# Optimization experiments

Hardware: AMD Instinct MI355X
Metric: run time of the kernel (lower is better)

Reference implementation:

```python
import jax, jax.numpy as jnp
import numpy as np

B, T, D = 64, 512, 1536   # batch, time, enc_size (2*768)
H = 30                    # z_rnn_size
L_SUP, R_SUP = -0.1, 1.1  # HardKuma stretched support
EPS = 1e-5


def setup_inputs() -> dict:
    key = jax.random.key(0)
    ks = jax.random.split(key, 12)
    s = 0.02
    return {
        "x": jax.random.normal(ks[0], (B, T, D), dtype=jnp.float32),
        "u": jax.random.uniform(ks[1], (B, T, 1), dtype=jnp.float32),
        # LSTMCell(enc_size + 1 -> H), torch gate order [i, f, g, o]
        "Wih": jax.random.normal(ks[2], (4 * H, D + 1), dtype=jnp.float32) * s,
        "Whh": jax.random.normal(ks[3], (4 * H, H), dtype=jnp.float32) * s,
        "bih": jax.random.normal(ks[4], (4 * H,), dtype=jnp.float32) * s,
        "bhh": jax.random.normal(ks[5], (4 * H,), dtype=jnp.float32) * s,
        # KumaGate: Linear(D + H -> 1) + Softplus for a and b
        "Wa": jax.random.normal(ks[6], (1, D + H), dtype=jnp.float32) * s,
        "ba": jax.random.normal(ks[7], (1,), dtype=jnp.float32) * s,
        "Wb": jax.random.normal(ks[8], (1, D + H), dtype=jnp.float32) * s,
        "bb": jax.random.normal(ks[9], (1,), dtype=jnp.float32) * s,
    }


def reference(x, u, Wih, Whh, bih, bhh, Wa, ba, Wb, bb):
    # x: [B, T, D], u: [B, T, 1] uniform reparam noise
    hseq = jnp.swapaxes(x, 0, 1)               # [T, B, D]
    useq = jnp.swapaxes(u, 0, 1)               # [T, B, 1]
    batch = x.shape[0]

    def step(carry, inp):
        hx, cx = carry                          # [B, H] each
        h_t, u_t = inp                          # [B, D], [B, 1]
        feat = jnp.concatenate([h_t, hx], axis=-1)          # [B, D+H]
        a = jnp.clip(jax.nn.softplus(feat @ Wa.T + ba), 1e-6, 100.0)
        b = jnp.clip(jax.nn.softplus(feat @ Wb.T + bb), 1e-6, 100.0)
        # HardKuma reparameterized sample (training branch)
        uu = jnp.clip(u_t, EPS, 1.0 - EPS)
        s = (1.0 - (1.0 - uu) ** (1.0 / b)) ** (1.0 / a)     # Kuma icdf
        t = s * (R_SUP - L_SUP) + L_SUP                      # stretch
        z_t = jnp.clip(t, 0.0, 1.0)                          # hard rectify, [B, 1]
        # LSTMCell update (torch gate order i, f, g, o)
        rnn_in = jnp.concatenate([h_t, z_t], axis=-1)        # [B, D+1]
        gates = rnn_in @ Wih.T + bih + hx @ Whh.T + bhh      # [B, 4H]
        i, f, g, o = jnp.split(gates, 4, axis=-1)
        c_new = jax.nn.sigmoid(f) * cx + jax.nn.sigmoid(i) * jnp.tanh(g)
        h_new = jax.nn.sigmoid(o) * jnp.tanh(c_new)
        return (h_new, c_new), z_t

    init = (jnp.zeros((batch, H), x.dtype), jnp.zeros((batch, H), x.dtype))
    _, zs = jax.lax.scan(step, init, (hseq, useq))           # zs: [T, B, 1]
    return jnp.swapaxes(zs[..., 0], 0, 1)                    # [B, T]
```

## Files before the change

### kernel.cpp

```cpp
#include <hip/hip_runtime.h>
#include <math.h>

#define Bb 64
#define Tt 512
#define Dd 1536
#define Hh 30
#define NC 128
#define Mm (Bb*Tt)
#define KSTEPS 48

typedef unsigned short u16;
typedef __attribute__((ext_vector_type(8))) short short8v;
typedef __attribute__((ext_vector_type(4))) float f32x4;

__device__ __forceinline__ float rcpf_(float x) { return __builtin_amdgcn_rcpf(x); }
__device__ __forceinline__ float sigmoidf_(float x) {
    return rcpf_(1.f + __expf(-x));
}
__device__ __forceinline__ float tanhf_fast(float x) {
    float e = __expf(2.f * x);
    return fmaf(-2.f, rcpf_(e + 1.f), 1.f);
}
__device__ __forceinline__ float softplus_(float x) {
    return fmaxf(x, 0.f) + __logf(1.f + __expf(-fabsf(x)));
}
__device__ __forceinline__ float rl_f(float v, int lane) {
    return __uint_as_float(__builtin_amdgcn_readlane(__float_as_uint(v), lane));
}

#define QPERM(src, CTRL) \
    __uint_as_float((unsigned)__builtin_amdgcn_mov_dpp((int)__float_as_uint(src), CTRL, 0xF, 0xF, false))

__device__ __forceinline__ f32x4 mm_bf16(short8v a, short8v b, f32x4 c) {
    return __builtin_amdgcn_mfma_f32_16x16x32_bf16(a, b, c, 0, 0, 0);
}

union U4S8 { unsigned int u[4]; short8v s; };

__device__ __forceinline__ void cvt_split(const float4 a, const float4 b,
                                          short8v& hi, short8v& lo) {
    float x[8] = {a.x, a.y, a.z, a.w, b.x, b.y, b.z, b.w};
    U4S8 H, L;
#pragma unroll
    for (int i = 0; i < 4; i++) {
        unsigned int u0 = __float_as_uint(x[2 * i]);
        unsigned int u1 = __float_as_uint(x[2 * i + 1]);
        unsigned int h0 = u0 & 0xffff0000u;
        unsigned int h1 = u1 & 0xffff0000u;
        H.u[i] = (u0 >> 16) | h1;
        float l0 = x[2 * i]     - __uint_as_float(h0);
        float l1 = x[2 * i + 1] - __uint_as_float(h1);
        L.u[i] = (__float_as_uint(l0) >> 16) | (__float_as_uint(l1) & 0xffff0000u);
    }
    hi = H.s;
    lo = L.s;
}

__global__ __launch_bounds__(256) void pack_w(const float* __restrict__ Wih,
                                              const float* __restrict__ Wa,
                                              const float* __restrict__ Wb,
                                              u16* __restrict__ Wbh,
                                              u16* __restrict__ Wbl) {
    const int k = blockIdx.x * 256 + threadIdx.x;
    const int c = blockIdx.y;
    float v = 0.f;
    if (c < 120)       v = Wih[c * (Dd + 1) + k];
    else if (c == 120) v = Wa[k];
    else if (c == 121) v = Wb[k];
    unsigned int u = __float_as_uint(v);
    unsigned int h = u & 0xffff0000u;
    float lo = v - __uint_as_float(h);
    Wbh[(size_t)c * Dd + k] = (u16)(u >> 16);
    Wbl[(size_t)c * Dd + k] = (u16)(__float_as_uint(lo) >> 16);
}

__global__ __launch_bounds__(64) void pack_s3(const float* __restrict__ Wih,
                                              const float* __restrict__ Whh,
                                              const float* __restrict__ Wa,
                                              const float* __restrict__ Wb,
                                              float* __restrict__ WS3) {
    const int l = threadIdx.x;
    const int q = l >> 2, g = l & 3;
    float v0[32], v1[32];
#pragma unroll
    for (int j = 0; j < 32; j++) { v0[j] = 0.f; v1[j] = 0.f; }
    {
        int c0 = g * 30 + q;
        for (int j = 0; j < 30; j++) v0[j] = Whh[c0 * Hh + j];
        v0[30] = Wih[c0 * (Dd + 1) + Dd];
    }
    if (q < 14) {
        int c1 = g * 30 + 16 + q;
        for (int j = 0; j < 30; j++) v1[j] = Whh[c1 * Hh + j];
        v1[30] = Wih[c1 * (Dd + 1) + Dd];
    } else if (l == 56) {
        for (int j = 0; j < 30; j++) v1[j] = Wa[Dd + j];
    } else if (l == 60) {
        for (int j = 0; j < 30; j++) v1[j] = Wb[Dd + j];
    }
    float* dst = WS3 + (size_t)l * 64;
    for (int j = 0; j < 32; j++) { dst[j] = v0[j]; dst[32 + j] = v1[j]; }
}

__global__ __launch_bounds__(256, 2) void gemm_k(const float* __restrict__ X,
                                                 const u16* __restrict__ Wbh,
                                                 const u16* __restrict__ Wbl,
                                                 const float* __restrict__ bih,
                                                 const float* __restrict__ bhh,
                                                 const float* __restrict__ ba,
                                                 const float* __restrict__ bbp,
                                                 float* __restrict__ GX) {
    const int t    = threadIdx.x;
    const int lane = t & 63;
    const int wid  = t >> 6;
    const int wrow = wid >> 1;
    const int wcol = wid & 1;
    const int m0   = blockIdx.x * 64 + wrow * 32;
    const int n0   = wcol * 64;
    const int lr   = lane & 15;
    const int lk   = lane >> 4;

    const float* xa0 = X + (size_t)(m0 + lr) * Dd + lk * 8;
    const float* xa1 = xa0 + (size_t)16 * Dd;
    const u16*   pbh = Wbh + (size_t)(n0 + lr) * Dd + lk * 8;
    const u16*   pbl = Wbl + (size_t)(n0 + lr) * Dd + lk * 8;

    f32x4 acc[2][4];
#pragma unroll
    for (int nt = 0; nt < 4; nt++) {
        int c = n0 + nt * 16 + lr;
        float bv = (c < 120) ? (bih[c] + bhh[c])
                 : (c == 120) ? ba[0]
                 : (c == 121) ? bbp[0] : 0.f;
        f32x4 v = {bv, bv, bv, bv};
        acc[0][nt] = v;
        acc[1][nt] = v;
    }

#define LOADA(ra, ks) do {                                        \
        ra[0] = *(const float4*)(xa0 + (ks) * 32);                \
        ra[1] = *(const float4*)(xa0 + (ks) * 32 + 4);            \
        ra[2] = *(const float4*)(xa1 + (ks) * 32);                \
        ra[3] = *(const float4*)(xa1 + (ks) * 32 + 4);            \
    } while (0)

#define LOADB(bh, bl, ks) do {                                               \
        _Pragma("unroll")                                                    \
        for (int nt = 0; nt < 4; nt++) {                                     \
            bh[nt] = *(const short8v*)(pbh + (size_t)nt * 16 * Dd + (ks) * 32); \
            bl[nt] = *(const short8v*)(pbl + (size_t)nt * 16 * Dd + (ks) * 32); \
        }                                                                    \
    } while (0)

#define STEP(ra, bh, bl) do {                                     \
        short8v ah0, al0, ah1, al1;                               \
        cvt_split(ra[0], ra[1], ah0, al0);                        \
        cvt_split(ra[2], ra[3], ah1, al1);                        \
        _Pragma("unroll")                                         \
        for (int nt = 0; nt < 4; nt++)                            \
            acc[0][nt] = mm_bf16(ah0, bh[nt], acc[0][nt]);        \
        _Pragma("unroll")                                         \
        for (int nt = 0; nt < 4; nt++)                            \
            acc[1][nt] = mm_bf16(ah1, bh[nt], acc[1][nt]);        \
        _Pragma("unroll")                                         \
        for (int nt = 0; nt < 4; nt++)                            \
            acc[0][nt] = mm_bf16(al0, bh[nt], acc[0][nt]);        \
        _Pragma("unroll")                                         \
        for (int nt = 0; nt < 4; nt++)                            \
            acc[1][nt] = mm_bf16(al1, bh[nt], acc[1][nt]);        \
        _Pragma("unroll")                                         \
        for (int nt = 0; nt < 4; nt++)                            \
            acc[0][nt] = mm_bf16(ah0, bl[nt], acc[0][nt]);        \
        _Pragma("unroll")                                         \
        for (int nt = 0; nt < 4; nt++)                            \
            acc[1][nt] = mm_bf16(ah1, bl[nt], acc[1][nt]);        \
    } while (0)

    float4  ra0[4], ra1[4];
    short8v bh0[4], bl0[4], bh1[4], bl1[4];

    LOADA(ra0, 0);
    LOADB(bh0, bl0, 0);
    int ks = 0;
    for (; ks < KSTEPS - 2; ks += 2) {
        LOADA(ra1, ks + 1);
        LOADB(bh1, bl1, ks + 1);
        STEP(ra0, bh0, bl0);
        LOADA(ra0, ks + 2);
        LOADB(bh0, bl0, ks + 2);
        STEP(ra1, bh1, bl1);
    }
    LOADA(ra1, KSTEPS - 1);
    LOADB(bh1, bl1, KSTEPS - 1);
    STEP(ra0, bh0, bl0);
    STEP(ra1, bh1, bl1);

#undef LOADA
#undef LOADB
#undef STEP

#pragma unroll
    for (int mt = 0; mt < 2; mt++)
#pragma unroll
        for (int nt = 0; nt < 4; nt++) {
            float* dst = GX + (size_t)(m0 + mt * 16 + lk * 4) * NC + n0 + nt * 16 + lr;
#pragma unroll
            for (int r = 0; r < 4; r++)
                dst[(size_t)r * NC] = acc[mt][nt][r];
        }
}

#define PIN16(A, B) asm volatile("" \
    : "+v"(A[B+0]), "+v"(A[B+1]), "+v"(A[B+2]),  "+v"(A[B+3]),  "+v"(A[B+4]),  "+v"(A[B+5]),  "+v"(A[B+6]),  "+v"(A[B+7]), \
      "+v"(A[B+8]), "+v"(A[B+9]), "+v"(A[B+10]), "+v"(A[B+11]), "+v"(A[B+12]), "+v"(A[B+13]), "+v"(A[B+14]), "+v"(A[B+15]))

__global__
__attribute__((amdgpu_flat_work_group_size(64, 64)))
__attribute__((amdgpu_waves_per_eu(1)))
void scan_k(const float* __restrict__ u,
            const float* __restrict__ gx,
            const float* __restrict__ WS3,
            float* __restrict__ out) {
    __shared__ float lus[Tt];
    __shared__ float zbuf[Tt];
    const int b = blockIdx.x;
    const int l = threadIdx.x;
    const int q = l >> 2, g = l & 3;

    for (int k = l; k < Tt; k += 64) {
        float uu = u[b * Tt + k];
        uu = fminf(fmaxf(uu, 1e-5f), 1.f - 1e-5f);
        lus[k] = __logf(1.f - uu);
    }
    __syncthreads();

    float wv0[32], wv1[32];
    {
        const float* wp = WS3 + (size_t)l * 64;
#pragma unroll
        for (int j = 0; j < 8; j++) {
            float4 a4 = ((const float4*)wp)[j];
            float4 b4 = ((const float4*)(wp + 32))[j];
            wv0[4 * j + 0] = a4.x; wv0[4 * j + 1] = a4.y;
            wv0[4 * j + 2] = a4.z; wv0[4 * j + 3] = a4.w;
            wv1[4 * j + 0] = b4.x; wv1[4 * j + 1] = b4.y;
            wv1[4 * j + 2] = b4.z; wv1[4 * j + 3] = b4.w;
        }
    }

    const int c0 = g * 30 + q;
    const int c1 = (q < 14) ? (g * 30 + 16 + q) : ((l == 56) ? 120 : (l == 60) ? 121 : 124);
    const float* p0 = gx + (size_t)b * Tt * NC + c0;
    const float* p1 = gx + (size_t)b * Tt * NC + c1;

    float hs[Hh];
#pragma unroll
    for (int k = 0; k < Hh; k++) hs[k] = 0.f;
    float cst0 = 0.f, cst1 = 0.f;

    float A0 = p0[0], B0 = p1[0];
    float A1 = p0[NC], B1 = p1[NC];
    float lu0 = lus[0], lu1 = lus[1];

    for (int t = 0; t < Tt; t++) {
        PIN16(wv0, 0); PIN16(wv0, 16);
        PIN16(wv1, 0); PIN16(wv1, 16);

        float d10 = B0, d11 = 0.f, d12 = 0.f, d13 = 0.f;
#pragma unroll
        for (int k = 0; k < 28; k += 4) {
            d10 = fmaf(wv1[k], hs[k], d10);         d11 = fmaf(wv1[k + 1], hs[k + 1], d11);
            d12 = fmaf(wv1[k + 2], hs[k + 2], d12); d13 = fmaf(wv1[k + 3], hs[k + 3], d13);
        }
        d10 = fmaf(wv1[28], hs[28], d10); d11 = fmaf(wv1[29], hs[29], d11);
        float dot1 = (d10 + d12) + (d11 + d13);

        const float av = rl_f(dot1, 56);
        const float bv = rl_f(dot1, 60);
        float a  = fminf(fmaxf(softplus_(av), 1e-6f), 100.f);
        float bk = fminf(fmaxf(softplus_(bv), 1e-6f), 100.f);
        float lu = lu0;
        float p = __expf(lu * rcpf_(bk));
        float inner = 1.f - p;
        float s = (inner <= 0.f) ? 0.f : __expf(__logf(inner) * rcpf_(a));
        float z = fminf(fmaxf(fmaf(1.2f, s, -0.1f), 0.f), 1.f);

        float d00 = A0, d01 = 0.f, d02 = 0.f, d03 = 0.f;
#pragma unroll
        for (int k = 0; k < 28; k += 4) {
            d00 = fmaf(wv0[k], hs[k], d00);         d01 = fmaf(wv0[k + 1], hs[k + 1], d01);
            d02 = fmaf(wv0[k + 2], hs[k + 2], d02); d03 = fmaf(wv0[k + 3], hs[k + 3], d03);
        }
        d00 = fmaf(wv0[28], hs[28], d00); d01 = fmaf(wv0[29], hs[29], d01);
        float dot0 = (d00 + d02) + (d01 + d03);

        A0 = A1; B0 = B1; lu0 = lu1;
        if (t + 2 < Tt) {
            A1 = p0[(size_t)(t + 2) * NC];
            B1 = p1[(size_t)(t + 2) * NC];
            lu1 = lus[t + 2];
        }

        float acc0 = fmaf(z, wv0[30], dot0);
        float acc1 = fmaf(z, wv1[30], dot1);

        float val0 = (g == 2) ? tanhf_fast(acc0) : sigmoidf_(acc0);
        float val1 = (g == 2) ? tanhf_fast(acc1) : sigmoidf_(acc1);

        float vf0 = QPERM(val0, 0x55), vg0 = QPERM(val0, 0xAA), vo0 = QPERM(val0, 0xFF);
        float vf1 = QPERM(val1, 0x55), vg1 = QPERM(val1, 0xAA), vo1 = QPERM(val1, 0xFF);

        float cn0 = fmaf(vf0, cst0, val0 * vg0);
        float hn0 = vo0 * tanhf_fast(cn0);
        cst0 = cn0;
        float cn1 = fmaf(vf1, cst1, val1 * vg1);
        float hn1 = vo1 * tanhf_fast(cn1);
        cst1 = cn1;

#pragma unroll
        for (int k = 0; k < 16; k++) hs[k] = rl_f(hn0, 4 * k);
#pragma unroll
        for (int k = 16; k < Hh; k++) hs[k] = rl_f(hn1, 4 * (k - 16));

        if (l == 0) zbuf[t] = z;
    }
    __syncthreads();
    for (int k = l; k < Tt; k += 64) out[b * Tt + k] = zbuf[k];
}

extern "C" void kernel_launch(void* const* d_in, const int* in_sizes, int n_in,
                              void* d_out, int out_size, void* d_ws, size_t ws_size,
                              hipStream_t stream) {
    const float* x   = (const float*)d_in[0];
    const float* u   = (const float*)d_in[1];
    const float* Wih = (const float*)d_in[2];
    const float* Whh = (const float*)d_in[3];
    const float* bih = (const float*)d_in[4];
    const float* bhh = (const float*)d_in[5];
    const float* Wa  = (const float*)d_in[6];
    const float* ba  = (const float*)d_in[7];
    const float* Wb  = (const float*)d_in[8];
    const float* bbp = (const float*)d_in[9];
    float* out = (float*)d_out;

    char* wsb = (char*)d_ws;
    u16*   Wbh = (u16*)(wsb);
    u16*   Wbl = (u16*)(wsb + 393216);
    float* WS3 = (float*)(wsb + 786432);
    float* GX  = (float*)(wsb + 802816);

    pack_w<<<dim3(Dd / 256, NC), 256, 0, stream>>>(Wih, Wa, Wb, Wbh, Wbl);
    pack_s3<<<1, 64, 0, stream>>>(Wih, Whh, Wa, Wb, WS3);
    gemm_k<<<Mm / 64, 256, 0, stream>>>(x, Wbh, Wbl, bih, bhh, ba, bbp, GX);
    scan_k<<<Bb, 64, 0, stream>>>(u, GX, WS3, out);
}
```

Baseline: 666.4 us.

## Stream gate projections into LDS in double-buffered chunks via async global_load_lds

The recurrent scan kernel used to issue scattered per-step global loads of the precomputed gate inputs, two steps ahead. It now copies 32-timestep chunks of the gate projections into a double-buffered shared-memory tile with asynchronous global-to-LDS loads, so each step reads from LDS with short latency. The per-step gate activation is also merged into one exp-plus-reciprocal path, with a per-lane multiplier selecting between sigmoid and tanh. This costs 32KB of LDS and a full vmcnt wait at each chunk boundary, and there is no barrier between the async LDS write and the reads, which relies on a single-wave workgroup.

```diff
diff --git a/kernel.cpp b/kernel.cpp
--- a/kernel.cpp
+++ b/kernel.cpp
@@ -30,6 +30,10 @@
 
 #define QPERM(src, CTRL) \
     __uint_as_float((unsigned)__builtin_amdgcn_mov_dpp((int)__float_as_uint(src), CTRL, 0xF, 0xF, false))
+
+#define GLOAD_LDS16(gp, lp) \
+    __builtin_amdgcn_global_load_lds((const __attribute__((address_space(1))) void*)(const void*)(gp), \
+                                     (__attribute__((address_space(3))) void*)(void*)(lp), 16, 0, 0)
 
 __device__ __forceinline__ f32x4 mm_bf16(short8v a, short8v b, f32x4 c) {
     return __builtin_amdgcn_mfma_f32_16x16x32_bf16(a, b, c, 0, 0, 0);
@@ -223,6 +227,7 @@
             float* __restrict__ out) {
     __shared__ float lus[Tt];
     __shared__ float zbuf[Tt];
+    __shared__ float gxs[2][32][NC];
     const int b = blockIdx.x;
     const int l = threadIdx.x;
     const int q = l >> 2, g = l & 3;
@@ -250,79 +255,104 @@
 
     const int c0 = g * 30 + q;
     const int c1 = (q < 14) ? (g * 30 + 16 + q) : ((l == 56) ? 120 : (l == 60) ? 121 : 124);
-    const float* p0 = gx + (size_t)b * Tt * NC + c0;
-    const float* p1 = gx + (size_t)b * Tt * NC + c1;
+    const float* gxb0 = gx + (size_t)b * Tt * NC;
+
+    const float mge = (g == 2) ? 2.f : -1.f;
 
     float hs[Hh];
 #pragma unroll
     for (int k = 0; k < Hh; k++) hs[k] = 0.f;
     float cst0 = 0.f, cst1 = 0.f;
 
-    float A0 = p0[0], B0 = p1[0];
-    float A1 = p0[NC], B1 = p1[NC];
-    float lu0 = lus[0], lu1 = lus[1];
-
-    for (int t = 0; t < Tt; t++) {
-        PIN16(wv0, 0); PIN16(wv0, 16);
-        PIN16(wv1, 0); PIN16(wv1, 16);
-
-        float d10 = B0, d11 = 0.f, d12 = 0.f, d13 = 0.f;
-#pragma unroll
-        for (int k = 0; k < 28; k += 4) {
-            d10 = fmaf(wv1[k], hs[k], d10);         d11 = fmaf(wv1[k + 1], hs[k + 1], d11);
-            d12 = fmaf(wv1[k + 2], hs[k + 2], d12); d13 = fmaf(wv1[k + 3], hs[k + 3], d13);
+#pragma unroll
+    for (int j = 0; j < 16; j++)
+        GLOAD_LDS16(gxb0 + j * 256 + l * 4, &gxs[0][0][0] + j * 256);
+    asm volatile("s_waitcnt vmcnt(0)" ::: "memory");
+    float A0 = gxs[0][0][c0], B0 = gxs[0][0][c1], L0 = lus[0];
+
+    for (int c = 0; c < Tt / 32; c++) {
+        if (c < Tt / 32 - 1) {
+            const float* gch = gxb0 + (size_t)(c + 1) * 32 * NC;
+            float* lch = &gxs[(c + 1) & 1][0][0];
+#pragma unroll
+            for (int j = 0; j < 16; j++)
+                GLOAD_LDS16(gch + j * 256 + l * 4, lch + j * 256);
         }
-        d10 = fmaf(wv1[28], hs[28], d10); d11 = fmaf(wv1[29], hs[29], d11);
-        float dot1 = (d10 + d12) + (d11 + d13);
-
-        const float av = rl_f(dot1, 56);
-        const float bv = rl_f(dot1, 60);
-        float a  = fminf(fmaxf(softplus_(av), 1e-6f), 100.f);
-        float bk = fminf(fmaxf(softplus_(bv), 1e-6f), 100.f);
-        float lu = lu0;
-        float p = __expf(lu * rcpf_(bk));
-        float inner = 1.f - p;
-        float s = (inner <= 0.f) ? 0.f : __expf(__logf(inner) * rcpf_(a));
-        float z = fminf(fmaxf(fmaf(1.2f, s, -0.1f), 0.f), 1.f);
-
-        float d00 = A0, d01 = 0.f, d02 = 0.f, d03 = 0.f;
-#pragma unroll
-        for (int k = 0; k < 28; k += 4) {
-            d00 = fmaf(wv0[k], hs[k], d00);         d01 = fmaf(wv0[k + 1], hs[k + 1], d01);
-            d02 = fmaf(wv0[k + 2], hs[k + 2], d02); d03 = fmaf(wv0[k + 3], hs[k + 3], d03);
+#pragma unroll 1
+        for (int s = 0; s < 32; s++) {
+            const int t = c * 32 + s;
+            PIN16(wv0, 0); PIN16(wv0, 16);
+            PIN16(wv1, 0); PIN16(wv1, 16);
+
+            float A1 = 0.f, B1 = 0.f, L1 = 0.f;
+            if (t + 1 < Tt) {
+                if (s < 31) {
+                    A1 = gxs[c & 1][s + 1][c0];
+                    B1 = gxs[c & 1][s + 1][c1];
+                } else {
+                    asm volatile("s_waitcnt vmcnt(0)" ::: "memory");
+                    A1 = gxs[(c + 1) & 1][0][c0];
+                    B1 = gxs[(c + 1) & 1][0][c1];
+                }
+                L1 = lus[t + 1];
+            }
+
+            float d10 = B0, d11 = 0.f, d12 = 0.f, d13 = 0.f;
+#pragma unroll
+            for (int k = 0; k < 28; k += 4) {
+                d10 = fmaf(wv1[k], hs[k], d10);         d11 = fmaf(wv1[k + 1], hs[k + 1], d11);
+                d12 = fmaf(wv1[k + 2], hs[k + 2], d12); d13 = fmaf(wv1[k + 3], hs[k + 3], d13);
+            }
+            d10 = fmaf(wv1[28], hs[28], d10); d11 = fmaf(wv1[29], hs[29], d11);
+            float dot1 = (d10 + d12) + (d11 + d13);
+
+            const float av = rl_f(dot1, 56);
+            const float bv = rl_f(dot1, 60);
+            float a  = fminf(fmaxf(softplus_(av), 1e-6f), 100.f);
+            float bk = fminf(fmaxf(softplus_(bv), 1e-6f), 100.f);
+            float lu = L0;
+            float p = __expf(lu * rcpf_(bk));
+            float inner = 1.f - p;
+            float sK = (inner <= 0.f) ? 0.f : __expf(__logf(inner) * rcpf_(a));
+            float z = fminf(fmaxf(fmaf(1.2f, sK, -0.1f), 0.f), 1.f);
+
+            float d00 = A0, d01 = 0.f, d02 = 0.f, d03 = 0.f;
+#pragma unroll
+            for (int k = 0; k < 28; k += 4) {
+                d00 = fmaf(wv0[k], hs[k], d00);         d01 = fmaf(wv0[k + 1], hs[k + 1], d01);
+                d02 = fmaf(wv0[k + 2], hs[k + 2], d02); d03 = fmaf(wv0[k + 3], hs[k + 3], d03);
+            }
+            d00 = fmaf(wv0[28], hs[28], d00); d01 = fmaf(wv0[29], hs[29], d01);
+            float dot0 = (d00 + d02) + (d01 + d03);
+
+            float acc0 = fmaf(z, wv0[30], dot0);
+            float acc1 = fmaf(z, wv1[30], dot1);
+
+            float e0 = __expf(acc0 * mge);
+            float e1 = __expf(acc1 * mge);
+            float r0 = rcpf_(1.f + e0);
+            float r1 = rcpf_(1.f + e1);
+            float val0 = (g == 2) ? fmaf(-2.f, r0, 1.f) : r0;
+            float val1 = (g == 2) ? fmaf(-2.f, r1, 1.f) : r1;
+
+            float vf0 = QPERM(val0, 0x55), vg0 = QPERM(val0, 0xAA), vo0 = QPERM(val0, 0xFF);
+            float vf1 = QPERM(val1, 0x55), vg1 = QPERM(val1, 0xAA), vo1 = QPERM(val1, 0xFF);
+
+            float cn0 = fmaf(vf0, cst0, val0 * vg0);
+            float hn0 = vo0 * tanhf_fast(cn0);
+            cst0 = cn0;
+            float cn1 = fmaf(vf1, cst1, val1 * vg1);
+            float hn1 = vo1 * tanhf_fast(cn1);
+            cst1 = cn1;
+
+#pragma unroll
+            for (int k = 0; k < 16; k++) hs[k] = rl_f(hn0, 4 * k);
+#pragma unroll
+            for (int k = 16; k < Hh; k++) hs[k] = rl_f(hn1, 4 * (k - 16));
+
+            if (l == 0) zbuf[t] = z;
+            A0 = A1; B0 = B1; L0 = L1;
         }
-        d00 = fmaf(wv0[28], hs[28], d00); d01 = fmaf(wv0[29], hs[29], d01);
-        float dot0 = (d00 + d02) + (d01 + d03);
-
-        A0 = A1; B0 = B1; lu0 = lu1;
-        if (t + 2 < Tt) {
-            A1 = p0[(size_t)(t + 2) * NC];
-            B1 = p1[(size_t)(t + 2) * NC];
-            lu1 = lus[t + 2];
-        }
-
-        float acc0 = fmaf(z, wv0[30], dot0);
-        float acc1 = fmaf(z, wv1[30], dot1);
-
-        float val0 = (g == 2) ? tanhf_fast(acc0) : sigmoidf_(acc0);
-        float val1 = (g == 2) ? tanhf_fast(acc1) : sigmoidf_(acc1);
-
-        float vf0 = QPERM(val0, 0x55), vg0 = QPERM(val0, 0xAA), vo0 = QPERM(val0, 0xFF);
-        float vf1 = QPERM(val1, 0x55), vg1 = QPERM(val1, 0xAA), vo1 = QPERM(val1, 0xFF);
-
-        float cn0 = fmaf(vf0, cst0, val0 * vg0);
-        float hn0 = vo0 * tanhf_fast(cn0);
-        cst0 = cn0;
-        float cn1 = fmaf(vf1, cst1, val1 * vg1);
-        float hn1 = vo1 * tanhf_fast(cn1);
-        cst1 = cn1;
-
-#pragma unroll
-        for (int k = 0; k < 16; k++) hs[k] = rl_f(hn0, 4 * k);
-#pragma unroll
-        for (int k = 16; k < Hh; k++) hs[k] = rl_f(hn1, 4 * (k - 16));
-
-        if (l == 0) zbuf[t] = z;
     }
     __syncthreads();
     for (int k = l; k < Tt; k += 64) out[b * Tt + k] = zbuf[k];
```

Result: faster. 649.5 us (-2.5%).
